# Kernel optimization log

Hardware: AMD Instinct MI355X
Metric: run time of the kernel (lower is better)

Reference implementation:

```python
import jax, jax.numpy as jnp
import numpy as np

A = -0.75  # torch grid_sample bicubic coefficient
EPS_CLAMP = 1e-07


def geo_pad(x, p):
    # GeoCyclicPadding: flip+half-roll across poles (H), circular in longitude (W)
    B, C, H, W = x.shape
    top = jnp.roll(jnp.flip(x[:, :, :p, :], axis=2), W // 2, axis=3)
    bot = jnp.roll(jnp.flip(x[:, :, H - p:, :], axis=2), W // 2, axis=3)
    x = jnp.concatenate([top, x, bot], axis=2)
    return jnp.concatenate([x[:, :, :, W - p:], x, x[:, :, :, :p]], axis=3)


def conv3(x, w, b):
    y = jax.lax.conv_general_dilated(x, w, (1, 1), 'VALID',
                                     dimension_numbers=('NCHW', 'OIHW', 'NCHW'))
    return y + b[None, :, None, None]


def layernorm_chw(x, g, b):
    mu = jnp.mean(x, axis=(1, 2, 3), keepdims=True)
    var = jnp.mean((x - mu) ** 2, axis=(1, 2, 3), keepdims=True)
    return (x - mu) * jax.lax.rsqrt(var + 1e-5) * g[None] + b[None]


def cubic_weights(t):
    # cubic convolution weights for taps at offsets -1,0,1,2 (a = -0.75)
    w0 = A * (1 + t) ** 3 - 5 * A * (1 + t) ** 2 + 8 * A * (1 + t) - 4 * A
    w1 = (A + 2) * t ** 3 - (A + 3) * t ** 2 + 1
    w2 = (A + 2) * (1 - t) ** 3 - (A + 3) * (1 - t) ** 2 + 1
    w3 = A * (2 - t) ** 3 - 5 * A * (2 - t) ** 2 + 8 * A * (2 - t) - 4 * A
    return (w0, w1, w2, w3)


def bicubic_sample_border(img, gx, gy):
    # img: [N,Hp,Wp]; gx,gy: [N,H,W] normalized coords; align_corners=True, border padding
    N, Hp, Wp = img.shape
    ix = jnp.clip((gx + 1) * 0.5 * (Wp - 1), 0.0, Wp - 1)
    iy = jnp.clip((gy + 1) * 0.5 * (Hp - 1), 0.0, Hp - 1)
    x0f = jnp.floor(ix)
    y0f = jnp.floor(iy)
    tx = ix - x0f
    ty = iy - y0f
    x0 = x0f.astype(jnp.int32)
    y0 = y0f.astype(jnp.int32)
    wx = cubic_weights(tx)
    wy = cubic_weights(ty)
    nidx = jnp.arange(N)[:, None, None]
    out = jnp.zeros_like(ix)
    for i in range(4):
        yi = jnp.clip(y0 + (i - 1), 0, Hp - 1)
        row = jnp.zeros_like(ix)
        for j in range(4):
            xj = jnp.clip(x0 + (j - 1), 0, Wp - 1)
            row = row + wx[j] * img[nidx, yi, xj]
        out = out + wy[i] * row
    return out


def reference(hidden_features, lat_grid, lon_grid, w1, b1, ln_g, ln_b, w2, b2, dt):
    B, C, H, W = hidden_features.shape
    # velocity_net = CLP (double conv)
    x = geo_pad(hidden_features, 1)
    x = conv3(x, w1, b1)
    x = jax.nn.silu(layernorm_chw(x, ln_g, ln_b))
    x = geo_pad(x, 1)
    vel = conv3(x, w2, b2)                      # [B, 2C, H, W]
    vel = vel.reshape(B, 2, C, H, W).transpose(0, 2, 1, 3, 4)  # [B, C, 2, H, W]
    u = vel[:, :, 0]
    v = vel[:, :, 1]
    lon_prime = -u * dt
    lat_prime = -v * dt
    lat_p = lat_grid[:, None, :, :]  # broadcast over channels
    lon_p = lon_grid[:, None, :, :]
    # rotated -> standard lat/lon
    sin_lat_prime = jnp.sin(lat_prime)
    cos_lat_prime = jnp.cos(lat_prime)
    sin_lon_prime = jnp.sin(lon_prime)
    cos_lon_prime = jnp.cos(lon_prime)
    sin_lat_p = jnp.sin(lat_p)
    cos_lat_p = jnp.cos(lat_p)
    sin_lat = sin_lat_prime * cos_lat_p + cos_lat_prime * cos_lon_prime * sin_lat_p
    lat_dep = jnp.arcsin(jnp.clip(sin_lat, -1 + EPS_CLAMP, 1 - EPS_CLAMP))
    num = cos_lat_prime * sin_lon_prime
    den = cos_lat_prime * cos_lon_prime * cos_lat_p - sin_lat_prime * sin_lat_p
    lon_dep = lon_p + jnp.arctan2(num, den)
    lon_dep = jnp.remainder(lon_dep + 2 * jnp.pi, 2 * jnp.pi)
    pw = W + 2
    ph = H + 2
    grid_x = (lon_dep / (2 * jnp.pi) * 2 - 1) * (W / pw)
    grid_y = (lat_dep / jnp.pi * 2 - 1) * (H / ph)
    padded = geo_pad(hidden_features, 1).reshape(B * C, ph, pw)
    out = bicubic_sample_border(padded,
                                grid_x.reshape(B * C, H, W),
                                grid_y.reshape(B * C, H, W))
    return out.reshape(B, C, H, W)


def setup_inputs() -> dict:
    key = jax.random.key(0)
    ks = jax.random.split(key, 4)
    B, C, H, W = 2, 128, 240, 480
    hidden_features = jax.random.normal(ks[0], (B, C, H, W), dtype=jnp.float32)
    lat = jnp.linspace(-jnp.pi / 2 + 1e-3, jnp.pi / 2 - 1e-3, H, dtype=jnp.float32)
    lon = jnp.linspace(0.0, 2 * jnp.pi * (1 - 1.0 / W), W, dtype=jnp.float32)
    lat_grid = jnp.broadcast_to(lat[None, :, None], (B, H, W)).astype(jnp.float32)
    lon_grid = jnp.broadcast_to(lon[None, None, :], (B, H, W)).astype(jnp.float32)
    w1 = jax.random.normal(ks[1], (C, C, 3, 3), dtype=jnp.float32) * 0.02
    b1 = jnp.zeros((C,), dtype=jnp.float32)
    ln_g = jnp.ones((C, H, W), dtype=jnp.float32)
    ln_b = jnp.zeros((C, H, W), dtype=jnp.float32)
    w2 = jax.random.normal(ks[2], (2 * C, C, 3, 3), dtype=jnp.float32) * 0.02
    b2 = jnp.zeros((2 * C,), dtype=jnp.float32)
    return {"hidden_features": hidden_features, "lat_grid": lat_grid,
            "lon_grid": lon_grid, "w1": w1, "b1": b1, "ln_g": ln_g,
            "ln_b": ln_b, "w2": w2, "b2": b2, "dt": 0.1}
```

## Files before the change

### kernel.cpp

```cpp
#include <hip/hip_runtime.h>
#include <math.h>

#define Hh 240
#define Ww 480
#define HW 115200
#define Cc 128
#define Kk 1152
#define HALFW 240
#define NB_RED 1440
#define WLCAP 4194304

typedef unsigned int u32;
typedef unsigned short u16;
typedef short bf16x8 __attribute__((ext_vector_type(8)));
typedef float f32x4 __attribute__((ext_vector_type(4)));
typedef __attribute__((address_space(3))) u32 lds_u32;
typedef const __attribute__((address_space(1))) u32 glb_u32;

__device__ __forceinline__ u16 f2bf(float x) {
    u32 u = __float_as_uint(x);
    u32 r = (u + 0x7fffu + ((u >> 16) & 1u)) >> 16;
    return (u16)r;
}
__device__ __forceinline__ float bf2f(u16 h) { return __uint_as_float(((u32)h) << 16); }

__device__ __forceinline__ int geo_sidx(int r, int c) {
    int wv = (c < 0) ? (Ww - 1) : ((c >= Ww) ? 0 : c);
    int rr;
    if (r < 0)        { rr = 0;      wv = (wv >= HALFW) ? wv - HALFW : wv + HALFW; }
    else if (r >= Hh) { rr = Hh - 1; wv = (wv >= HALFW) ? wv - HALFW : wv + HALFW; }
    else              { rr = r; }
    return rr * Ww + wv;
}

__device__ __forceinline__ float padfetch(const float* __restrict__ p, int yi, int xj) {
    return p[geo_sidx(yi - 1, xj - 1)];
}

__device__ __forceinline__ void sincos_small(double x, double* s, double* c) {
    double x2 = x * x;
    if (x2 > 0.49) { *s = sin(x); *c = cos(x); return; }
    *s = x * (1.0 + x2 * (-1.6666666666666666e-1 + x2 * (8.3333333333333333e-3 +
         x2 * (-1.9841269841269841e-4 + x2 * (2.7557319223985893e-6 - x2 * 2.5052108385441720e-8)))));
    *c = 1.0 + x2 * (-0.5 + x2 * (4.1666666666666666e-2 + x2 * (-1.3888888888888889e-3 +
         x2 * (2.4801587301587302e-5 - x2 * 2.7557319223985893e-7))));
}

__device__ __forceinline__ void snipe_tail(double u, double v, double dt,
                                           double phi_s, double phi_c, double lam,
                                           const float* __restrict__ plane,
                                           float* __restrict__ outp)
{
    const double TWO_PI = 6.2831853071795864769252867665590;
    const double PI_D   = 3.1415926535897932384626433832795;

    double lonp = -u * dt, latp = -v * dt;
    double slp, clp, slo, clo;
    sincos_small(latp, &slp, &clp);
    sincos_small(lonp, &slo, &clo);

    double sinlat = slp * phi_c + clp * clo * phi_s;
    sinlat = fmin(fmax(sinlat, -1.0 + 1e-7), 1.0 - 1e-7);
    double lat_dep = asin(sinlat);

    double num = clp * slo;
    double den = clp * clo * phi_c - slp * phi_s;
    double lon_dep = lam + atan2(num, den);
    double xr = lon_dep + TWO_PI;
    xr = xr - floor(xr / TWO_PI) * TWO_PI;

    double gx = (xr / TWO_PI * 2.0 - 1.0) * (480.0 / 482.0);
    double gy = (lat_dep / PI_D * 2.0 - 1.0) * (240.0 / 242.0);
    double ixd = fmin(fmax((gx + 1.0) * 0.5 * 481.0, 0.0), 481.0);
    double iyd = fmin(fmax((gy + 1.0) * 0.5 * 241.0, 0.0), 241.0);

    double x0d = floor(ixd), y0d = floor(iyd);
    float fx = (float)(ixd - x0d), fy = (float)(iyd - y0d);
    int x0 = (int)x0d, y0 = (int)y0d;

    const float a = -0.75f;
    float wx[4], wy[4];
    {
        float t = fx;
        float t1 = 1.f + t, t2 = 2.f - t, s1 = 1.f - t;
        wx[0] = ((a * t1 - 5.f * a) * t1 + 8.f * a) * t1 - 4.f * a;
        wx[1] = ((a + 2.f) * t - (a + 3.f)) * t * t + 1.f;
        wx[2] = ((a + 2.f) * s1 - (a + 3.f)) * s1 * s1 + 1.f;
        wx[3] = ((a * t2 - 5.f * a) * t2 + 8.f * a) * t2 - 4.f * a;
        t = fy;
        t1 = 1.f + t; t2 = 2.f - t; s1 = 1.f - t;
        wy[0] = ((a * t1 - 5.f * a) * t1 + 8.f * a) * t1 - 4.f * a;
        wy[1] = ((a + 2.f) * t - (a + 3.f)) * t * t + 1.f;
        wy[2] = ((a + 2.f) * s1 - (a + 3.f)) * s1 * s1 + 1.f;
        wy[3] = ((a * t2 - 5.f * a) * t2 + 8.f * a) * t2 - 4.f * a;
    }
    float accv = 0.f;
    #pragma unroll
    for (int i = 0; i < 4; i++) {
        int yi = min(max(y0 + i - 1, 0), 241);
        float row = 0.f;
        #pragma unroll
        for (int j = 0; j < 4; j++) {
            int xj = min(max(x0 + j - 1, 0), 481);
            row = fmaf(wx[j], padfetch(plane, yi, xj), row);
        }
        accv = fmaf(wy[i], row, accv);
    }
    *outp = accv;
}

__global__ void reorder_w(const float* __restrict__ w, u16* __restrict__ outp, int NN) {
    int idx = blockIdx.x * 256 + threadIdx.x;
    int total = 3 * NN * Kk;
    if (idx >= total) return;
    int per_kt = 3 * NN * 32;
    int t = idx / per_kt;
    int rem = idx - t * per_kt;
    int U = rem >> 3, j = rem & 7;
    int NT64 = (NN / 16) * 64;
    int p = U / NT64;
    int r2 = U - p * NT64;
    int ntile = r2 >> 6, part = (r2 >> 4) & 3, nlow = r2 & 15;
    int n = ntile * 16 + nlow;
    int k = t * 32 + part * 8 + j;
    float x = w[(size_t)n * Kk + k];
    u16 a = f2bf(x); float r1 = x - bf2f(a);
    u16 b = f2bf(r1); float rr = r1 - bf2f(b);
    outp[idx] = (p == 0) ? a : ((p == 1) ? b : f2bf(rr));
}

template<int NN>
__global__ __launch_bounds__(512)
void conv_mfma(const float* __restrict__ in,
               const u16*  __restrict__ wspr,
               const float* __restrict__ bias,
               float* __restrict__ out)
{
    constexpr int NT     = NN / 64;
    constexpr int NTILES = NN / 16;
    __shared__ short Al[2][3][8][4][16][8];
    __shared__ short Bl[2][3][NTILES][4][16][8];

    const int tid  = threadIdx.x;
    const int lane = tid & 63;
    const int wave = tid >> 6;
    const int wm = wave & 1, wn = wave >> 1;
    const int lr = lane & 15, kg = lane >> 4;
    const int m0 = blockIdx.x * 128;

    const int ms   = tid & 127;
    const int grp  = tid >> 7;
    const int mt_s = ms >> 4, lr_s = ms & 15;
    const int gm = m0 + ms;
    const int h = gm / Ww, w = gm - h * Ww;
    int sidx[9];
    #pragma unroll
    for (int q = 0; q < 9; q++) sidx[q] = geo_sidx(h + q / 3 - 1, w + q % 3 - 1);

    constexpr int NCH = (3 * NN * 32 / 8) / 512;

    f32x4 acc[4][NT] = {};

    auto stageB = [&](int buf, int kt) {
        const u16* src = wspr + (size_t)(kt >> 5) * (3 * NN * 32) + (size_t)tid * 8;
        short* dst = &Bl[buf][0][0][0][0][0];
        #pragma unroll
        for (int cg = 0; cg < NCH; cg++) {
            __builtin_amdgcn_global_load_lds(
                (glb_u32*)(src + (size_t)cg * 4096),
                (lds_u32*)(dst + (size_t)(cg * 512 + tid) * 8), 16, 0, 0);
        }
    };
    auto loadA = [&](int kt, float* xv) {
        int k = kt + grp * 8;
        int ic = k / 9, t9 = k - ic * 9;
        #pragma unroll
        for (int j = 0; j < 8; j++) {
            xv[j] = in[ic * HW + sidx[t9]];
            if (++t9 == 9) { t9 = 0; ic++; }
        }
    };
    auto writeA = [&](int buf, const float* xv) {
        bf16x8 v0, v1, v2;
        #pragma unroll
        for (int j = 0; j < 8; j++) {
            float x = xv[j];
            u16 a = f2bf(x); float r1 = x - bf2f(a);
            u16 b = f2bf(r1); float r2 = r1 - bf2f(b);
            v0[j] = (short)a; v1[j] = (short)b; v2[j] = (short)f2bf(r2);
        }
        *(bf16x8*)&Al[buf][0][mt_s][grp][lr_s][0] = v0;
        *(bf16x8*)&Al[buf][1][mt_s][grp][lr_s][0] = v1;
        *(bf16x8*)&Al[buf][2][mt_s][grp][lr_s][0] = v2;
    };

    {
        float xv[8];
        stageB(0, 0);
        loadA(0, xv);
        writeA(0, xv);
    }

    int cur = 0;
    for (int kt = 0; kt < Kk; kt += 32) {
        __syncthreads();
        bf16x8 af[3][4];
        #pragma unroll
        for (int pa = 0; pa < 3; pa++)
            #pragma unroll
            for (int mt = 0; mt < 4; mt++)
                af[pa][mt] = *(const bf16x8*)&Al[cur][pa][wm * 4 + mt][kg][lr][0];

        float xv[8];
        const bool more = (kt + 32 < Kk);
        if (more) {
            stageB(cur ^ 1, kt + 32);
            loadA(kt + 32, xv);
        }

        #pragma unroll
        for (int pb = 0; pb < 3; pb++) {
            #pragma unroll
            for (int nt = 0; nt < NT; nt++) {
                bf16x8 bq = *(const bf16x8*)&Bl[cur][pb][wn * NT + nt][kg][lr][0];
                #pragma unroll
                for (int pa = 0; pa < 3 - pb; pa++)
                    #pragma unroll
                    for (int mt = 0; mt < 4; mt++)
                        acc[mt][nt] = __builtin_amdgcn_mfma_f32_16x16x32_bf16(
                            af[pa][mt], bq, acc[mt][nt], 0, 0, 0);
            }
        }
        if (more) writeA(cur ^ 1, xv);
        cur ^= 1;
    }

    #pragma unroll
    for (int mt = 0; mt < 4; mt++) {
        int mbase = m0 + wm * 64 + mt * 16 + kg * 4;
        #pragma unroll
        for (int nt = 0; nt < NT; nt++) {
            int n = wn * (NN / 4) + nt * 16 + lr;
            float bv = bias[n];
            float4 o;
            o.x = acc[mt][nt][0] + bv;
            o.y = acc[mt][nt][1] + bv;
            o.z = acc[mt][nt][2] + bv;
            o.w = acc[mt][nt][3] + bv;
            *(float4*)&out[(size_t)n * HW + mbase] = o;
        }
    }
}

__global__ __launch_bounds__(256)
void reduce_stats(const float* __restrict__ y, float* __restrict__ part) {
    const int n4 = (Cc * HW) / 4;
    float s = 0.f, ss = 0.f;
    for (int i = blockIdx.x * 256 + threadIdx.x; i < n4; i += NB_RED * 256) {
        float4 v = ((const float4*)y)[i];
        s  += v.x + v.y + v.z + v.w;
        ss += v.x * v.x + v.y * v.y + v.z * v.z + v.w * v.w;
    }
    #pragma unroll
    for (int o = 32; o > 0; o >>= 1) { s += __shfl_down(s, o); ss += __shfl_down(ss, o); }
    __shared__ float ls[4], lss[4];
    int wid = threadIdx.x >> 6, lane = threadIdx.x & 63;
    if (lane == 0) { ls[wid] = s; lss[wid] = ss; }
    __syncthreads();
    if (threadIdx.x == 0) {
        part[blockIdx.x * 2]     = ls[0] + ls[1] + ls[2] + ls[3];
        part[blockIdx.x * 2 + 1] = lss[0] + lss[1] + lss[2] + lss[3];
    }
}

__global__ __launch_bounds__(256)
void finalize_stats(const float* __restrict__ part, float* __restrict__ stats) {
    float s = 0.f, ss = 0.f;
    for (int i = threadIdx.x; i < NB_RED; i += 256) { s += part[2 * i]; ss += part[2 * i + 1]; }
    #pragma unroll
    for (int o = 32; o > 0; o >>= 1) { s += __shfl_down(s, o); ss += __shfl_down(ss, o); }
    __shared__ float ls[4], lss[4];
    int wid = threadIdx.x >> 6, lane = threadIdx.x & 63;
    if (lane == 0) { ls[wid] = s; lss[wid] = ss; }
    __syncthreads();
    if (threadIdx.x == 0) {
        stats[0] = ls[0] + ls[1] + ls[2] + ls[3];
        stats[1] = lss[0] + lss[1] + lss[2] + lss[3];
    }
}

__global__ void norm_silu(float* __restrict__ y, const float* __restrict__ g,
                          const float* __restrict__ bb, const float* __restrict__ stats) {
    int i = blockIdx.x * 256 + threadIdx.x;
    if (i >= Cc * HW) return;
    const float invN = 1.f / (float)(Cc * HW);
    float mu  = stats[0] * invN;
    float var = stats[1] * invN - mu * mu;
    float inv = rsqrtf(var + 1e-5f);
    float z = (y[i] - mu) * inv * g[i] + bb[i];
    y[i] = z / (1.f + expf(-z));
}

__global__ __launch_bounds__(256)
void semilag(const float* __restrict__ vel, const float* __restrict__ hid,
             const float* __restrict__ latg, const float* __restrict__ lng,
             const float* __restrict__ dtp, float* __restrict__ out,
             u32* __restrict__ wl, u32* __restrict__ wlcnt)
{
    int idx = blockIdx.x * 256 + threadIdx.x;
    if (idx >= Cc * HW) return;
    int c = idx / HW;
    int m = idx - c * HW;

    const float PI2F = 6.28318530717958647692f;

    float uf = vel[idx];
    float vf = vel[Cc * HW + idx];
    float dtf = dtp[0];
    float phi = latg[m], lam = lng[m];
    float sphi = sinf(phi), cphi = cosf(phi);

    float lonp = -uf * dtf, latp = -vf * dtf;
    float slp = sinf(latp), clp = cosf(latp);
    float slo = sinf(lonp), clo = cosf(lonp);
    float sinlat = slp * cphi + clp * clo * sphi;
    float num = clp * slo;
    float den = clp * clo * cphi - slp * sphi;
    float r2 = num * num + den * den;

    float lon_w = lam + atan2f(num, den) + PI2F;
    lon_w = lon_w - floorf(lon_w / PI2F) * PI2F;
    float seam = fminf(lon_w, PI2F - lon_w);

    bool pole = (m < 2 * Ww) | (m >= HW - 2 * Ww);
    bool snipe = !pole & ((r2 < 1e-4f) | (fabsf(sinlat) > 1.f - 1e-5f) | (seam < 1e-3f));
    if (snipe) {
        u32 s = atomicAdd(wlcnt, 1u);
        if (s < WLCAP) wl[s] = (u32)idx;
    }

    float sl = fminf(fmaxf(sinlat, -1.f + 1e-7f), 1.f - 1e-7f);
    float lat_dep = asinf(sl);
    float gx = (lon_w / PI2F * 2.f - 1.f) * (480.f / 482.f);
    float gy = (lat_dep / 3.14159265358979323846f * 2.f - 1.f) * (240.f / 242.f);
    double ixd = (double)fminf(fmaxf((gx + 1.f) * 0.5f * 481.f, 0.f), 481.f);
    double iyd = (double)fminf(fmaxf((gy + 1.f) * 0.5f * 241.f, 0.f), 241.f);

    double x0d = floor(ixd), y0d = floor(iyd);
    float fx = (float)(ixd - x0d), fy = (float)(iyd - y0d);
    int x0 = (int)x0d, y0 = (int)y0d;

    const float a = -0.75f;
    float wx[4], wy[4];
    {
        float t = fx;
        float t1 = 1.f + t, t2 = 2.f - t, s1 = 1.f - t;
        wx[0] = ((a * t1 - 5.f * a) * t1 + 8.f * a) * t1 - 4.f * a;
        wx[1] = ((a + 2.f) * t - (a + 3.f)) * t * t + 1.f;
        wx[2] = ((a + 2.f) * s1 - (a + 3.f)) * s1 * s1 + 1.f;
        wx[3] = ((a * t2 - 5.f * a) * t2 + 8.f * a) * t2 - 4.f * a;
        t = fy;
        t1 = 1.f + t; t2 = 2.f - t; s1 = 1.f - t;
        wy[0] = ((a * t1 - 5.f * a) * t1 + 8.f * a) * t1 - 4.f * a;
        wy[1] = ((a + 2.f) * t - (a + 3.f)) * t * t + 1.f;
        wy[2] = ((a + 2.f) * s1 - (a + 3.f)) * s1 * s1 + 1.f;
        wy[3] = ((a * t2 - 5.f * a) * t2 + 8.f * a) * t2 - 4.f * a;
    }

    const float* plane = hid + (size_t)c * HW;
    float accv = 0.f;
    #pragma unroll
    for (int i = 0; i < 4; i++) {
        int yi = min(max(y0 + i - 1, 0), 241);
        float row = 0.f;
        #pragma unroll
        for (int j = 0; j < 4; j++) {
            int xj = min(max(x0 + j - 1, 0), 481);
            row = fmaf(wx[j], padfetch(plane, yi, xj), row);
        }
        accv = fmaf(wy[i], row, accv);
    }
    out[idx] = accv;
}

__global__ __launch_bounds__(256)
void sniper_rows(const float* __restrict__ y1, const float* __restrict__ w2,
                 const float* __restrict__ b2, const float* __restrict__ hid,
                 const float* __restrict__ latg, const float* __restrict__ lng,
                 const float* __restrict__ dtp, float* __restrict__ out)
{
    __shared__ float xl[Kk];
    __shared__ double resd[256];

    const int tid = threadIdx.x;
    const int ri  = blockIdx.x / Ww;
    const int col = blockIdx.x - ri * Ww;
    const int r   = (ri < 2) ? ri : (236 + ri);
    const int m   = r * Ww + col;

    for (int k = tid; k < Kk; k += 256) {
        int ic = k / 9, t9 = k - ic * 9;
        xl[k] = y1[ic * HW + geo_sidx(r + t9 / 3 - 1, col + t9 % 3 - 1)];
    }
    __syncthreads();

    {
        const float* wrow = w2 + (size_t)tid * Kk;
        double a0 = 0.0, a1 = 0.0, a2 = 0.0, a3 = 0.0;
        #pragma unroll 4
        for (int k = 0; k < Kk; k += 4) {
            a0 = fma((double)wrow[k],     (double)xl[k],     a0);
            a1 = fma((double)wrow[k + 1], (double)xl[k + 1], a1);
            a2 = fma((double)wrow[k + 2], (double)xl[k + 2], a2);
            a3 = fma((double)wrow[k + 3], (double)xl[k + 3], a3);
        }
        resd[tid] = (a0 + a1) + (a2 + a3);
    }
    __syncthreads();

    if (tid < Cc) {
        double u = (double)b2[tid] + resd[tid];
        double v = (double)b2[Cc + tid] + resd[Cc + tid];
        double dt = (double)dtp[0];
        double phi = (double)latg[m];
        snipe_tail(u, v, dt, sin(phi), cos(phi), (double)lng[m],
                   hid + (size_t)tid * HW, &out[(size_t)tid * HW + m]);
    }
}

__global__ __launch_bounds__(256)
void sniper(const u32* __restrict__ wl, const u32* __restrict__ wlcnt,
            const float* __restrict__ y1, const float* __restrict__ w2,
            const float* __restrict__ b2, const float* __restrict__ hid,
            const float* __restrict__ latg, const float* __restrict__ lng,
            const float* __restrict__ dtp, float* __restrict__ out)
{
    const int lane = threadIdx.x & 63;
    const int wavid = (blockIdx.x * 256 + threadIdx.x) >> 6;
    const int nwaves = gridDim.x * 4;
    int n = (int)*wlcnt; if (n > WLCAP) n = WLCAP;

    for (int e = wavid; e < n; e += nwaves) {
        u32 idx = wl[e];
        int c = idx / HW, m = idx - c * HW;
        int h = m / Ww, w = m - h * Ww;

        double su = 0.0, sv = 0.0;
        const float* wu = w2 + (size_t)c * Kk;
        const float* wv = w2 + (size_t)(Cc + c) * Kk;
        #pragma unroll
        for (int t9 = 0; t9 < 9; t9++) {
            int s = geo_sidx(h + t9 / 3 - 1, w + t9 % 3 - 1);
            #pragma unroll
            for (int q = 0; q < 2; q++) {
                int ic = q * 64 + lane;
                int k = ic * 9 + t9;
                double yv = (double)y1[ic * HW + s];
                su = fma((double)wu[k], yv, su);
                sv = fma((double)wv[k], yv, sv);
            }
        }
        #pragma unroll
        for (int o = 32; o > 0; o >>= 1) {
            su += __shfl_down(su, o);
            sv += __shfl_down(sv, o);
        }
        if (lane == 0) {
            double u = (double)b2[c] + su;
            double v = (double)b2[Cc + c] + sv;
            double dt = (double)dtp[0];
            double phi = (double)latg[m];
            snipe_tail(u, v, dt, sin(phi), cos(phi), (double)lng[m],
                       hid + (size_t)c * HW, &out[idx]);
        }
    }
}

extern "C" void kernel_launch(void* const* d_in, const int* in_sizes, int n_in,
                              void* d_out, int out_size, void* d_ws, size_t ws_size,
                              hipStream_t stream)
{
    const float* hidden = (const float*)d_in[0];
    const float* latg   = (const float*)d_in[1];
    const float* lng    = (const float*)d_in[2];
    const float* w1     = (const float*)d_in[3];
    const float* b1     = (const float*)d_in[4];
    const float* g      = (const float*)d_in[5];
    const float* lb     = (const float*)d_in[6];
    const float* w2     = (const float*)d_in[7];
    const float* b2     = (const float*)d_in[8];
    const float* dt     = (const float*)d_in[9];
    float* out = (float*)d_out;

    float* ws    = (float*)d_ws;
    float* stats = ws;
    float* part  = ws + 4;
    u32*   wlcnt = (u32*)(ws + 4 + 2 * NB_RED);
    u16*   wsp1  = (u16*)(ws + 4 + 2 * NB_RED + 4);
    u16*   wsp2  = wsp1 + (size_t)3 * Cc * Kk;
    float* y1    = (float*)(wsp2 + (size_t)3 * 2 * Cc * Kk);
    float* vel   = y1 + (size_t)Cc * HW;
    u32*   wl    = (u32*)(vel + (size_t)2 * Cc * HW);

    reorder_w<<<(3 * Cc * Kk + 255) / 256, 256, 0, stream>>>(w1, wsp1, Cc);
    reorder_w<<<(3 * 2 * Cc * Kk + 255) / 256, 256, 0, stream>>>(w2, wsp2, 2 * Cc);

    for (int b = 0; b < 2; b++) {
        const float* hb = hidden + (size_t)b * Cc * HW;
        const float* lab = latg + (size_t)b * HW;
        const float* lob = lng + (size_t)b * HW;
        float* ob = out + (size_t)b * Cc * HW;

        conv_mfma<128><<<HW / 128, 512, 0, stream>>>(hb, wsp1, b1, y1);
        reduce_stats<<<NB_RED, 256, 0, stream>>>(y1, part);
        finalize_stats<<<1, 256, 0, stream>>>(part, stats + 2 * b);
        norm_silu<<<(Cc * HW) / 256, 256, 0, stream>>>(y1, g, lb, stats + 2 * b);
        conv_mfma<256><<<HW / 128, 512, 0, stream>>>(y1, wsp2, b2, vel);
        hipMemsetAsync(wlcnt, 0, 4, stream);
        semilag<<<(Cc * HW) / 256, 256, 0, stream>>>(vel, hb, lab, lob, dt, ob, wl, wlcnt);
        sniper_rows<<<4 * Ww, 256, 0, stream>>>(y1, w2, b2, hb, lab, lob, dt, ob);
        sniper<<<2048, 256, 0, stream>>>(wl, wlcnt, y1, w2, b2, hb, lab, lob, dt, ob);
    }
}
```

Before: 2.791 ms.

## Replace double-buffered conv K-loop with single-buffered load-sync-compute

Removes the LDS double buffering and software prefetch in the MFMA conv kernel. Each K step now loads the weight tile and gathered input tile, splits it into bf16 parts, syncs, then computes. This halves LDS use, which may allow more blocks per CU. The cost is that global loads no longer overlap with MFMA work and there is an extra barrier per iteration.

Result: faster. 2.694 ms (-3.5%).

```diff
diff --git a/kernel.cpp b/kernel.cpp
--- a/kernel.cpp
+++ b/kernel.cpp
@@ -138,8 +138,8 @@
 {
     constexpr int NT     = NN / 64;
     constexpr int NTILES = NN / 16;
-    __shared__ short Al[2][3][8][4][16][8];
-    __shared__ short Bl[2][3][NTILES][4][16][8];
+    __shared__ short Al[3][8][4][16][8];
+    __shared__ short Bl[3][NTILES][4][16][8];
 
     const int tid  = threadIdx.x;
     const int lane = tid & 63;
@@ -161,68 +161,53 @@
 
     f32x4 acc[4][NT] = {};
 
-    auto stageB = [&](int buf, int kt) {
-        const u16* src = wspr + (size_t)(kt >> 5) * (3 * NN * 32) + (size_t)tid * 8;
-        short* dst = &Bl[buf][0][0][0][0][0];
-        #pragma unroll
-        for (int cg = 0; cg < NCH; cg++) {
-            __builtin_amdgcn_global_load_lds(
-                (glb_u32*)(src + (size_t)cg * 4096),
-                (lds_u32*)(dst + (size_t)(cg * 512 + tid) * 8), 16, 0, 0);
-        }
-    };
-    auto loadA = [&](int kt, float* xv) {
-        int k = kt + grp * 8;
-        int ic = k / 9, t9 = k - ic * 9;
-        #pragma unroll
-        for (int j = 0; j < 8; j++) {
-            xv[j] = in[ic * HW + sidx[t9]];
-            if (++t9 == 9) { t9 = 0; ic++; }
-        }
-    };
-    auto writeA = [&](int buf, const float* xv) {
-        bf16x8 v0, v1, v2;
-        #pragma unroll
-        for (int j = 0; j < 8; j++) {
-            float x = xv[j];
-            u16 a = f2bf(x); float r1 = x - bf2f(a);
-            u16 b = f2bf(r1); float r2 = r1 - bf2f(b);
-            v0[j] = (short)a; v1[j] = (short)b; v2[j] = (short)f2bf(r2);
-        }
-        *(bf16x8*)&Al[buf][0][mt_s][grp][lr_s][0] = v0;
-        *(bf16x8*)&Al[buf][1][mt_s][grp][lr_s][0] = v1;
-        *(bf16x8*)&Al[buf][2][mt_s][grp][lr_s][0] = v2;
-    };
-
-    {
-        float xv[8];
-        stageB(0, 0);
-        loadA(0, xv);
-        writeA(0, xv);
-    }
-
-    int cur = 0;
     for (int kt = 0; kt < Kk; kt += 32) {
         __syncthreads();
+        {
+            const u16* src = wspr + (size_t)(kt >> 5) * (3 * NN * 32) + (size_t)tid * 8;
+            short* dst = &Bl[0][0][0][0][0];
+            #pragma unroll
+            for (int cg = 0; cg < NCH; cg++) {
+                __builtin_amdgcn_global_load_lds(
+                    (glb_u32*)(src + (size_t)cg * 4096),
+                    (lds_u32*)(dst + (size_t)(cg * 512 + tid) * 8), 16, 0, 0);
+            }
+        }
+        {
+            int k = kt + grp * 8;
+            int ic = k / 9, t9 = k - ic * 9;
+            float xv[8];
+            #pragma unroll
+            for (int j = 0; j < 8; j++) {
+                xv[j] = in[ic * HW + sidx[t9]];
+                if (++t9 == 9) { t9 = 0; ic++; }
+            }
+            bf16x8 v0, v1, v2;
+            #pragma unroll
+            for (int j = 0; j < 8; j++) {
+                float x = xv[j];
+                u16 a = f2bf(x); float r1 = x - bf2f(a);
+                u16 b = f2bf(r1); float r2 = r1 - bf2f(b);
+                v0[j] = (short)a; v1[j] = (short)b; v2[j] = (short)f2bf(r2);
+            }
+            *(bf16x8*)&Al[0][mt_s][grp][lr_s][0] = v0;
+            *(bf16x8*)&Al[1][mt_s][grp][lr_s][0] = v1;
+            *(bf16x8*)&Al[2][mt_s][grp][lr_s][0] = v2;
+        }
+        __syncthreads();
+
         bf16x8 af[3][4];
         #pragma unroll
         for (int pa = 0; pa < 3; pa++)
             #pragma unroll
             for (int mt = 0; mt < 4; mt++)
-                af[pa][mt] = *(const bf16x8*)&Al[cur][pa][wm * 4 + mt][kg][lr][0];
-
-        float xv[8];
-        const bool more = (kt + 32 < Kk);
-        if (more) {
-            stageB(cur ^ 1, kt + 32);
-            loadA(kt + 32, xv);
-        }
+                af[pa][mt] = *(const bf16x8*)&Al[pa][wm * 4 + mt][kg][lr][0];
 
         #pragma unroll
         for (int pb = 0; pb < 3; pb++) {
             #pragma unroll
             for (int nt = 0; nt < NT; nt++) {
-                bf16x8 bq = *(const bf16x8*)&Bl[cur][pb][wn * NT + nt][kg][lr][0];
+                bf16x8 bq = *(const bf16x8*)&Bl[pb][wn * NT + nt][kg][lr][0];
                 #pragma unroll
                 for (int pa = 0; pa < 3 - pb; pa++)
                     #pragma unroll
@@ -231,8 +216,6 @@
                             af[pa][mt], bq, acc[mt][nt], 0, 0, 0);
             }
         }
-        if (more) writeA(cur ^ 1, xv);
-        cur ^= 1;
     }
 
     #pragma unroll
```
